# Kernel optimization log

Measured on AMD Instinct MI355X. Metric: run time of the kernel, lower is better.

Reference implementation:

```python
import jax, jax.numpy as jnp
import numpy as np

G = 32               # sdf grid resolution (grid_size init default)
SCALE_FACTOR = 0.2   # forward default scale_factor
EPS = 1e-12


def setup_inputs() -> dict:
    key = jax.random.key(0)
    k1, k2 = jax.random.split(key)
    H, V, F = 2, 778, 1538  # two hands, MANO topology
    vertices = jax.random.normal(k1, (H, V, 3), dtype=jnp.float32)
    faces = jax.random.randint(k2, (F, 3), 0, V, dtype=jnp.int32)
    return {"vertices": vertices, "faces": faces}


def _sdiv(n, d):
    return n / jnp.where(jnp.abs(d) < EPS, EPS, d)


def _point_tri_dist2(p, a, b, c):
    # p: [P,1,3]; a,b,c: [1,F,3] -> squared distance [P,F] (Ericson closest-point)
    ab = b - a; ac = c - a; ap = p - a
    d1 = jnp.sum(ab * ap, -1); d2 = jnp.sum(ac * ap, -1)
    bp = p - b; d3 = jnp.sum(ab * bp, -1); d4 = jnp.sum(ac * bp, -1)
    cp = p - c; d5 = jnp.sum(ab * cp, -1); d6 = jnp.sum(ac * cp, -1)
    vc = d1 * d4 - d3 * d2
    vb = d5 * d2 - d1 * d6
    va = d3 * d6 - d5 * d4
    denom = va + vb + vc
    v_in = _sdiv(vb, denom); w_in = _sdiv(vc, denom)
    res = a + ab * v_in[..., None] + ac * w_in[..., None]  # face interior
    # edge BC
    cond = ((va <= 0) & ((d4 - d3) >= 0) & ((d5 - d6) >= 0))[..., None]
    w = _sdiv(d4 - d3, (d4 - d3) + (d5 - d6))[..., None]
    res = jnp.where(cond, b + (c - b) * w, res)
    # edge AC
    cond = ((vb <= 0) & (d2 >= 0) & (d6 <= 0))[..., None]
    w = _sdiv(d2, d2 - d6)[..., None]
    res = jnp.where(cond, a + ac * w, res)
    # edge AB
    cond = ((vc <= 0) & (d1 >= 0) & (d3 <= 0))[..., None]
    w = _sdiv(d1, d1 - d3)[..., None]
    res = jnp.where(cond, a + ab * w, res)
    # vertex regions (highest precedence)
    res = jnp.where(((d6 >= 0) & (d5 <= d6))[..., None], jnp.broadcast_to(c, res.shape), res)
    res = jnp.where(((d3 >= 0) & (d4 <= d3))[..., None], jnp.broadcast_to(b, res.shape), res)
    res = jnp.where(((d1 <= 0) & (d2 <= 0))[..., None], jnp.broadcast_to(a, res.shape), res)
    return jnp.sum((p - res) ** 2, -1)


def _inside(p, a, b, c):
    # parity of +x ray intersections (Moller-Trumbore with dir = (1,0,0))
    e1 = b - a; e2 = c - a
    det = e1[..., 1] * (-e2[..., 2]) + e1[..., 2] * e2[..., 1]  # dot(e1, cross(dir,e2))
    inv = _sdiv(1.0, det)
    s = p - a
    u = (s[..., 1] * (-e2[..., 2]) + s[..., 2] * e2[..., 1]) * inv
    q = jnp.cross(s, e1)
    v = q[..., 0] * inv                # dot(dir, q)
    t = jnp.sum(e2 * q, -1) * inv
    hit = (jnp.abs(det) > 1e-9) & (u >= 0) & (u <= 1) & (v >= 0) & (u + v <= 1) & (t > 0)
    return (jnp.sum(hit.astype(jnp.int32), axis=-1) % 2) == 1


def _sdf_grid(tri):
    # tri: [F,3,3] scaled triangles -> phi [G,G,G] laid out [z,y,x] (grid_sample DHW)
    a = tri[None, :, 0]; b = tri[None, :, 1]; c = tri[None, :, 2]
    lin = jnp.linspace(-1.0, 1.0, G, dtype=tri.dtype)
    zz, yy, xx = jnp.meshgrid(lin, lin, lin, indexing='ij')
    pts = jnp.stack([xx, yy, zz], -1).reshape(G, G * G, 3)  # chunk over z-slabs

    def slab(ps):
        p = ps[:, None, :]
        d2 = jnp.min(_point_tri_dist2(p, a, b, c), axis=1)
        ins = _inside(p, a, b, c)
        return jnp.where(ins, jnp.sqrt(jnp.maximum(d2, 0.0)), 0.0)

    return jax.lax.map(slab, pts).reshape(G, G, G)


def _trilinear(phi, coords):
    # grid_sample(align_corners=True, padding_mode='zeros'), coords [N,3] in xyz order
    g = G - 1
    f = (coords + 1.0) * 0.5 * g
    fx, fy, fz = f[:, 0], f[:, 1], f[:, 2]
    x0f = jnp.floor(fx); y0f = jnp.floor(fy); z0f = jnp.floor(fz)
    wx = fx - x0f; wy = fy - y0f; wz = fz - z0f
    x0 = x0f.astype(jnp.int32); y0 = y0f.astype(jnp.int32); z0 = z0f.astype(jnp.int32)

    def corner(zi, yi, xi, w):
        valid = (zi >= 0) & (zi <= g) & (yi >= 0) & (yi <= g) & (xi >= 0) & (xi <= g)
        val = phi[jnp.clip(zi, 0, g), jnp.clip(yi, 0, g), jnp.clip(xi, 0, g)]
        return jnp.where(valid, val, 0.0) * w

    out = (corner(z0, y0, x0, (1 - wz) * (1 - wy) * (1 - wx))
           + corner(z0, y0, x0 + 1, (1 - wz) * (1 - wy) * wx)
           + corner(z0, y0 + 1, x0, (1 - wz) * wy * (1 - wx))
           + corner(z0, y0 + 1, x0 + 1, (1 - wz) * wy * wx)
           + corner(z0 + 1, y0, x0, wz * (1 - wy) * (1 - wx))
           + corner(z0 + 1, y0, x0 + 1, wz * (1 - wy) * wx)
           + corner(z0 + 1, y0 + 1, x0, wz * wy * (1 - wx))
           + corner(z0 + 1, y0 + 1, x0 + 1, wz * wy * wx))
    return out


def reference(vertices, faces):
    H = vertices.shape[0]
    bmin = vertices.min(axis=1)   # [H,3]
    bmax = vertices.max(axis=1)
    center = jax.lax.stop_gradient(((bmin + bmax) * 0.5)[:, None, :])           # [H,1,3]
    scale = jax.lax.stop_gradient(
        ((1.0 + SCALE_FACTOR) * 0.5 * (bmax - bmin).max(-1))[:, None, None])    # [H,1,1]
    v_scaled = jax.lax.stop_gradient((vertices - center) / scale)
    tris = v_scaled[:, faces]                                                    # [H,F,3,3]
    phi = jax.lax.stop_gradient(jax.vmap(_sdf_grid)(tris))                       # [H,G,G,G]
    i = 1  # hardcoded loop 'for i in [1]' in the source
    coords = ((vertices - center[i][None]) / scale[i][None]).reshape(-1, 3)
    phi_val = _trilinear(phi[i], coords).reshape(H, -1)
    weights = jnp.ones((H, 1), dtype=vertices.dtype).at[i, 0].set(0.0)
    loss = jnp.sum(weights * phi_val) / (H ** 2)
    return loss
```

## Files before the change

### kernel.cpp

```cpp
#include <hip/hip_runtime.h>
#include <math.h>

#define NNODE 32768
#define NTHR  256
#define STHR  1024
#define CH    256
#define MAXC  (CH + 63)
#define FGRID 2048
#define NL1   64
#define CREW  8

__device__ __forceinline__ float rguard(float d) {
    float dd = (fabsf(d) < 1e-12f) ? 1e-12f : d;
    return __builtin_amdgcn_rcpf(dd);
}

__device__ __forceinline__ void cell_of(float px, float py, float pz,
                                        int& x0, int& y0, int& z0,
                                        float& wx, float& wy, float& wz) {
#pragma clang fp contract(off)
    float fx = (px + 1.0f) * 0.5f * 31.0f;
    float fy = (py + 1.0f) * 0.5f * 31.0f;
    float fz = (pz + 1.0f) * 0.5f * 31.0f;
    float x0f = floorf(fx), y0f = floorf(fy), z0f = floorf(fz);
    wx = fx - x0f; wy = fy - y0f; wz = fz - z0f;
    x0 = (int)fmaxf(fminf(x0f, 33.0f), -2.0f);
    y0 = (int)fmaxf(fminf(y0f, 33.0f), -2.0f);
    z0 = (int)fmaxf(fminf(z0f, 33.0f), -2.0f);
}

__device__ __forceinline__ void bbox_of(const float* __restrict__ verts, int V,
                                        float& ocx, float& ocy, float& ocz,
                                        float& osc) {
#pragma clang fp contract(off)
    const float* v1 = verts + (size_t)V * 3;
    float mn[3] = {1e30f, 1e30f, 1e30f};
    float mx[3] = {-1e30f, -1e30f, -1e30f};
    for (int i = threadIdx.x; i < V; i += blockDim.x) {
        for (int c = 0; c < 3; ++c) {
            float val = v1[i * 3 + c];
            mn[c] = fminf(mn[c], val);
            mx[c] = fmaxf(mx[c], val);
        }
    }
    for (int off = 32; off >= 1; off >>= 1) {
        for (int c = 0; c < 3; ++c) {
            mn[c] = fminf(mn[c], __shfl_down(mn[c], off));
            mx[c] = fmaxf(mx[c], __shfl_down(mx[c], off));
        }
    }
    __shared__ float smn[16][3], smx[16][3];
    int wv = threadIdx.x >> 6, lane = threadIdx.x & 63;
    if (lane == 0)
        for (int c = 0; c < 3; ++c) { smn[wv][c] = mn[c]; smx[wv][c] = mx[c]; }
    __syncthreads();
    const int nw = (int)blockDim.x >> 6;
    float ext = -1e30f, cc[3];
    for (int c = 0; c < 3; ++c) {
        float lo = 1e30f, hi = -1e30f;
        for (int w = 0; w < nw; ++w) {
            lo = fminf(lo, smn[w][c]);
            hi = fmaxf(hi, smx[w][c]);
        }
        cc[c] = (lo + hi) * 0.5f;
        ext = fmaxf(ext, hi - lo);
    }
    ocx = cc[0]; ocy = cc[1]; ocz = cc[2];
    osc = (1.0f + 0.2f) * 0.5f * ext;
    __syncthreads();
}

__device__ __forceinline__ void tri_node(
        float ax, float ay, float az, float abx, float aby, float abz,
        float acx, float acy, float acz, float inv, float det,
        float dbb, float dbc, float dcc,
        float px, float py, float pz, float& mind2, int& h) {
    float apx = px - ax, apy = py - ay, apz = pz - az;
    {
#pragma clang fp contract(fast)
        float d1 = abx * apx + aby * apy + abz * apz;
        float d2 = acx * apx + acy * apy + acz * apz;
        float d3 = d1 - dbb;
        float d4 = d2 - dbc;
        float d5 = d1 - dbc;
        float d6 = d2 - dcc;
        float vc = d1 * d4 - d3 * d2;
        float vb = d5 * d2 - d1 * d6;
        float va = d3 * d6 - d5 * d4;
        float denom = va + vb + vc;
        float rd = rguard(denom);
        float v_in = vb * rd, w_in = vc * rd;
        float rx = ax + abx * v_in + acx * w_in;
        float ry = ay + aby * v_in + acy * w_in;
        float rz = az + abz * v_in + acz * w_in;
        if (va <= 0.0f && (d4 - d3) >= 0.0f && (d5 - d6) >= 0.0f) {
            float w2 = (d4 - d3) * rguard((d4 - d3) + (d5 - d6));
            rx = ax + abx + (acx - abx) * w2;
            ry = ay + aby + (acy - aby) * w2;
            rz = az + abz + (acz - abz) * w2;
        }
        if (vb <= 0.0f && d2 >= 0.0f && d6 <= 0.0f) {
            float w2 = d2 * rguard(d2 - d6);
            rx = ax + acx * w2; ry = ay + acy * w2; rz = az + acz * w2;
        }
        if (vc <= 0.0f && d1 >= 0.0f && d3 <= 0.0f) {
            float w2 = d1 * rguard(d1 - d3);
            rx = ax + abx * w2; ry = ay + aby * w2; rz = az + abz * w2;
        }
        if (d6 >= 0.0f && d5 <= d6) { rx = ax + acx; ry = ay + acy; rz = az + acz; }
        if (d3 >= 0.0f && d4 <= d3) { rx = ax + abx; ry = ay + aby; rz = az + abz; }
        if (d1 <= 0.0f && d2 <= 0.0f) { rx = ax; ry = ay; rz = az; }
        float ddx = px - rx, ddy = py - ry, ddz = pz - rz;
        mind2 = fminf(mind2, ddx * ddx + ddy * ddy + ddz * ddz);
    }
    {
#pragma clang fp contract(off)
        float u = (apy * (-acz) + apz * acy) * inv;
        float qx = apy * abz - apz * aby;
        float qy = apz * abx - apx * abz;
        float qz = apx * aby - apy * abx;
        float v = qx * inv;
        float tt = (acx * qx + acy * qy + acz * qz) * inv;
        h += (fabsf(det) > 1e-9f && u >= 0.0f && u <= 1.0f && v >= 0.0f &&
              (u + v) <= 1.0f && tt > 0.0f) ? 1 : 0;
    }
}

__global__ void __launch_bounds__(STHR) k_setup(
        const float* __restrict__ verts, const int* __restrict__ faces,
        float* __restrict__ tri, unsigned int* __restrict__ d2b,
        int* __restrict__ hits, int* __restrict__ cnt,
        unsigned long long* __restrict__ acc, int* __restrict__ done2,
        int* __restrict__ lvl1, int* __restrict__ lvl2,
        int* __restrict__ list, int V, int F) {
    float cx0, cy0, cz0, sc;
    bbox_of(verts, V, cx0, cy0, cz0, sc);
    const int b = (int)blockIdx.x, tid = threadIdx.x;

    if (b == 0) {
        __shared__ unsigned bm[NNODE / 32];
        __shared__ int scnt[STHR];
        bm[tid] = 0u;
        __syncthreads();
        for (int i = tid; i < V; i += STHR) {
#pragma clang fp contract(off)
            float px = (verts[i * 3 + 0] - cx0) / sc;
            float py = (verts[i * 3 + 1] - cy0) / sc;
            float pz = (verts[i * 3 + 2] - cz0) / sc;
            int x0, y0, z0; float wx, wy, wz;
            cell_of(px, py, pz, x0, y0, z0, wx, wy, wz);
            for (int k = 0; k < 8; ++k) {
                int zi = z0 + ((k >> 2) & 1), yi = y0 + ((k >> 1) & 1),
                    xi = x0 + (k & 1);
                if ((unsigned)zi < 32u && (unsigned)yi < 32u && (unsigned)xi < 32u) {
                    int node = (zi * 32 + yi) * 32 + xi;
                    atomicOr(&bm[node >> 5], 1u << (node & 31));
                }
            }
        }
        __syncthreads();
        unsigned w0 = bm[tid];
        int c = __popc(w0);
        scnt[tid] = c;
        __syncthreads();
        for (int off = 1; off < STHR; off <<= 1) {
            int v_ = (tid >= off) ? scnt[tid - off] : 0;
            __syncthreads();
            scnt[tid] += v_;
            __syncthreads();
        }
        int total = scnt[STHR - 1];
        if (tid == STHR - 1) cnt[0] = total;
        int off = scnt[tid] - c;
        int basebit = tid * 32;
        while (w0) {
            int bb = __ffs(w0) - 1;
            list[off++] = basebit + bb;
            w0 &= w0 - 1;
        }
        __syncthreads();
        for (int t = tid; t < total; t += STHR) {
            int nd = list[t];
            d2b[nd] = 0xFFFFFFFFu;
            hits[nd] = 0;
        }
        if (tid < NL1) lvl1[tid * 16] = 0;
        if (tid == 0) { acc[0] = 0ull; done2[0] = 0; lvl2[0] = 0; }
    } else {
        int f = (b - 1) * STHR + tid;
        if (f < F) {
#pragma clang fp contract(off)
            const float* v1 = verts + (size_t)V * 3;
            int i0 = faces[f * 3 + 0], i1 = faces[f * 3 + 1], i2 = faces[f * 3 + 2];
            float ax = (v1[i0 * 3 + 0] - cx0) / sc, ay = (v1[i0 * 3 + 1] - cy0) / sc,
                  az = (v1[i0 * 3 + 2] - cz0) / sc;
            float bx = (v1[i1 * 3 + 0] - cx0) / sc, by = (v1[i1 * 3 + 1] - cy0) / sc,
                  bz = (v1[i1 * 3 + 2] - cz0) / sc;
            float cx = (v1[i2 * 3 + 0] - cx0) / sc, cy = (v1[i2 * 3 + 1] - cy0) / sc,
                  cz = (v1[i2 * 3 + 2] - cz0) / sc;
            float abx = bx - ax, aby = by - ay, abz = bz - az;
            float acx = cx - ax, acy = cy - ay, acz = cz - az;
            float det = aby * (-acz) + abz * acy;
            float dd = (fabsf(det) < 1e-12f) ? 1e-12f : det;
            float inv = 1.0f / dd;
            float* r = tri + (size_t)f * 16;
            r[0] = ax;  r[1] = ay;  r[2] = az;
            r[3] = abx; r[4] = aby; r[5] = abz;
            r[6] = acx; r[7] = acy; r[8] = acz;
            r[9] = inv; r[10] = det;
            r[11] = abx * abx + aby * aby + abz * abz;
            r[12] = abx * acx + aby * acy + abz * acz;
            r[13] = acx * acx + acy * acy + acz * acz;
            r[14] = 0.0f; r[15] = 0.0f;
        }
    }
}

__global__ void __launch_bounds__(NTHR) k_fused(
        const float* __restrict__ tri, const int* __restrict__ list,
        const int* __restrict__ cnt, unsigned int* __restrict__ d2b,
        int* __restrict__ hits, int* __restrict__ lvl1, int* __restrict__ lvl2,
        unsigned long long* __restrict__ acc, int* __restrict__ done2,
        const float* __restrict__ verts, float* __restrict__ out,
        int F, int nch, int V) {
    const int n = cnt[0];
    const int ngroups = (n + 3) >> 2;
    const int total = ngroups * nch;
    const int tid = threadIdx.x, lane = tid & 63;
    __shared__ float s[14][MAXC];

    for (int item = (int)blockIdx.x; item < total; item += FGRID) {
        const int group = item / nch;
        const int c = item - group * nch;
        const int cbase = c * CH;
        const int tn = (c == nch - 1) ? (F - cbase) : CH;

        for (int j = tid; j < tn; j += NTHR) {
            const float4* g = (const float4*)(tri + (size_t)(cbase + j) * 16);
            float4 r0 = g[0], r1 = g[1], r2 = g[2], r3 = g[3];
            s[0][j] = r0.x;  s[1][j] = r0.y;  s[2][j] = r0.z;  s[3][j] = r0.w;
            s[4][j] = r1.x;  s[5][j] = r1.y;  s[6][j] = r1.z;  s[7][j] = r1.w;
            s[8][j] = r2.x;  s[9][j] = r2.y;  s[10][j] = r2.z; s[11][j] = r2.w;
            s[12][j] = r3.x; s[13][j] = r3.y;
        }
        __syncthreads();

        const int idx = group * 4 + (tid >> 6);
        const int node = (idx < n) ? list[idx] : -1;
        float px = 0, py = 0, pz = 0;
        if (node >= 0) {
#pragma clang fp contract(off)
            px = (float)((double)(node & 31) * (2.0 / 31.0) - 1.0);
            py = (float)((double)((node >> 5) & 31) * (2.0 / 31.0) - 1.0);
            pz = (float)((double)(node >> 10) * (2.0 / 31.0) - 1.0);
        }
        float m = 1e30f;
        int h = 0;
        if (node >= 0) {
            for (int mi = 0; mi * 64 < tn; ++mi) {
                int j = lane + mi * 64;
                if (j < tn) {
                    tri_node(s[0][j], s[1][j], s[2][j], s[3][j], s[4][j], s[5][j],
                             s[6][j], s[7][j], s[8][j], s[9][j], s[10][j],
                             s[11][j], s[12][j], s[13][j], px, py, pz, m, h);
                }
            }
        }
        for (int off = 32; off >= 1; off >>= 1) {
            m = fminf(m, __shfl_xor(m, off));
            h += __shfl_xor(h, off);
        }
        if (lane == 0 && node >= 0) {
            atomicMin(d2b + node, __float_as_uint(m));
            atomicAdd(hits + node, h);
        }
        __syncthreads();
    }

    __shared__ int crew_slice;
    __syncthreads();
    if (tid == 0) {
        crew_slice = -1;
        int cohort = (int)blockIdx.x & (NL1 - 1);
        int quota = (FGRID + NL1 - 1 - cohort) / NL1;
        int p1 = atomicAdd(&lvl1[cohort * 16], 1);
        if (p1 == quota - 1) {
            int p2 = atomicAdd(lvl2, 1);
            if (p2 >= NL1 - CREW) {
                while (__hip_atomic_load(lvl2, __ATOMIC_RELAXED,
                                         __HIP_MEMORY_SCOPE_AGENT) < NL1)
                    __builtin_amdgcn_s_sleep(1);
                crew_slice = p2 - (NL1 - CREW);
            }
        }
    }
    __syncthreads();
    const int slice = crew_slice;
    if (slice < 0) return;

    float cx, cy, cz, sc;
    bbox_of(verts, V, cx, cy, cz, sc);
    float val = 0.0f;
    {
#pragma clang fp contract(off)
        for (int i = slice * NTHR + tid; i < V; i += CREW * NTHR) {
            float px = (verts[i * 3 + 0] - cx) / sc;
            float py = (verts[i * 3 + 1] - cy) / sc;
            float pz = (verts[i * 3 + 2] - cz) / sc;
            int x0, y0, z0; float wx, wy, wz;
            cell_of(px, py, pz, x0, y0, z0, wx, wy, wz);
            auto corner = [&](int zi, int yi, int xi, float w) -> float {
#pragma clang fp contract(off)
                bool valid = (zi >= 0) && (zi <= 31) && (yi >= 0) && (yi <= 31) &&
                             (xi >= 0) && (xi <= 31);
                int zc = min(max(zi, 0), 31);
                int yc = min(max(yi, 0), 31);
                int xc = min(max(xi, 0), 31);
                int idx = (zc * 32 + yc) * 32 + xc;
                unsigned dbits = __hip_atomic_load(&d2b[idx], __ATOMIC_RELAXED,
                                                   __HIP_MEMORY_SCOPE_AGENT);
                int hh = __hip_atomic_load(&hits[idx], __ATOMIC_RELAXED,
                                           __HIP_MEMORY_SCOPE_AGENT);
                float vv = (hh & 1) ? sqrtf(fmaxf(__uint_as_float(dbits), 0.0f))
                                    : 0.0f;
                return valid ? vv * w : 0.0f;
            };
            val += corner(z0, y0, x0, (1.0f - wz) * (1.0f - wy) * (1.0f - wx))
                 + corner(z0, y0, x0 + 1, (1.0f - wz) * (1.0f - wy) * wx)
                 + corner(z0, y0 + 1, x0, (1.0f - wz) * wy * (1.0f - wx))
                 + corner(z0, y0 + 1, x0 + 1, (1.0f - wz) * wy * wx)
                 + corner(z0 + 1, y0, x0, wz * (1.0f - wy) * (1.0f - wx))
                 + corner(z0 + 1, y0, x0 + 1, wz * (1.0f - wy) * wx)
                 + corner(z0 + 1, y0 + 1, x0, wz * wy * (1.0f - wx))
                 + corner(z0 + 1, y0 + 1, x0 + 1, wz * wy * wx);
        }
    }
    __shared__ float sm[NTHR];
    sm[tid] = val;
    __syncthreads();
    for (int ss = NTHR / 2; ss >= 1; ss >>= 1) {
        if (tid < ss) sm[tid] += sm[tid + ss];
        __syncthreads();
    }
    if (tid == 0) {
        unsigned long long fx =
            (unsigned long long)((double)sm[0] * 4294967296.0);
        atomicAdd(acc, fx);
        asm volatile("s_waitcnt vmcnt(0)");
        int prev = atomicAdd(done2, 1);
        if (prev == CREW - 1) {
            unsigned long long tot = atomicAdd(acc, 0ull);
            out[0] = (float)((double)tot / 4294967296.0 * 0.25);
        }
    }
}

extern "C" void kernel_launch(void* const* d_in, const int* in_sizes, int n_in,
                              void* d_out, int out_size, void* d_ws, size_t ws_size,
                              hipStream_t stream) {
    const float* verts = (const float*)d_in[0];
    const int* faces = (const int*)d_in[1];
    float* out = (float*)d_out;
    float* ws = (float*)d_ws;

    int V = in_sizes[0] / 6;
    int F = in_sizes[1] / 3;

    unsigned long long* acc = (unsigned long long*)ws;
    int* done2 = (int*)(ws + 2);
    int* cnt = (int*)(ws + 3);
    int* lvl2 = (int*)(ws + 4);
    int* lvl1 = (int*)(ws + 16);
    float* tri = ws + 16 + NL1 * 16;
    unsigned int* d2b = (unsigned int*)(tri + 16 * (size_t)F);
    int* hits = (int*)(d2b + NNODE);
    int* list = hits + NNODE;

    int nch = F / CH;
    int rem = F - nch * CH;
    if (nch == 0 || rem >= 64) nch += (rem > 0 ? 1 : 0);
    if (nch == 0) nch = 1;

    int nrec = (F + STHR - 1) / STHR;

    k_setup<<<1 + nrec, STHR, 0, stream>>>(verts, faces, tri, d2b, hits, cnt, acc,
                                           done2, lvl1, lvl2, list, V, F);
    k_fused<<<FGRID, NTHR, 0, stream>>>(tri, list, cnt, d2b, hits, lvl1, lvl2, acc,
                                        done2, verts, out, F, nch, V);
}
```

Measured before the change: 43.99 us.

## Compute point-triangle distance algebraically from dot products and defer atomics

```diff
diff --git a/kernel.cpp b/kernel.cpp
--- a/kernel.cpp
+++ b/kernel.cpp
@@ -72,7 +72,7 @@
 
 __device__ __forceinline__ void tri_node(
         float ax, float ay, float az, float abx, float aby, float abz,
-        float acx, float acy, float acz, float inv, float det,
+        float acx, float acy, float acz, float inv, float ebc,
         float dbb, float dbc, float dcc,
         float px, float py, float pz, float& mind2, int& h) {
     float apx = px - ax, apy = py - ay, apz = pz - az;
@@ -80,6 +80,7 @@
 #pragma clang fp contract(fast)
         float d1 = abx * apx + aby * apy + abz * apz;
         float d2 = acx * apx + acy * apy + acz * apz;
+        float apd = apx * apx + apy * apy + apz * apz;
         float d3 = d1 - dbb;
         float d4 = d2 - dbc;
         float d5 = d1 - dbc;
@@ -89,29 +90,26 @@
         float va = d3 * d6 - d5 * d4;
         float denom = va + vb + vc;
         float rd = rguard(denom);
-        float v_in = vb * rd, w_in = vc * rd;
-        float rx = ax + abx * v_in + acx * w_in;
-        float ry = ay + aby * v_in + acy * w_in;
-        float rz = az + abz * v_in + acz * w_in;
+        float v = vb * rd, w = vc * rd;
+        float dd = apd - 2.0f * (v * d1 + w * d2) + v * v * dbb +
+                   2.0f * v * w * dbc + w * w * dcc;
         if (va <= 0.0f && (d4 - d3) >= 0.0f && (d5 - d6) >= 0.0f) {
             float w2 = (d4 - d3) * rguard((d4 - d3) + (d5 - d6));
-            rx = ax + abx + (acx - abx) * w2;
-            ry = ay + aby + (acy - aby) * w2;
-            rz = az + abz + (acz - abz) * w2;
+            dd = apd - 2.0f * d1 + dbb - 2.0f * w2 * (d2 - d1) +
+                 2.0f * w2 * (dbc - dbb) + w2 * w2 * ebc;
         }
         if (vb <= 0.0f && d2 >= 0.0f && d6 <= 0.0f) {
             float w2 = d2 * rguard(d2 - d6);
-            rx = ax + acx * w2; ry = ay + acy * w2; rz = az + acz * w2;
+            dd = apd - 2.0f * w2 * d2 + w2 * w2 * dcc;
         }
         if (vc <= 0.0f && d1 >= 0.0f && d3 <= 0.0f) {
             float w2 = d1 * rguard(d1 - d3);
-            rx = ax + abx * w2; ry = ay + aby * w2; rz = az + abz * w2;
-        }
-        if (d6 >= 0.0f && d5 <= d6) { rx = ax + acx; ry = ay + acy; rz = az + acz; }
-        if (d3 >= 0.0f && d4 <= d3) { rx = ax + abx; ry = ay + aby; rz = az + abz; }
-        if (d1 <= 0.0f && d2 <= 0.0f) { rx = ax; ry = ay; rz = az; }
-        float ddx = px - rx, ddy = py - ry, ddz = pz - rz;
-        mind2 = fminf(mind2, ddx * ddx + ddy * ddy + ddz * ddz);
+            dd = apd - 2.0f * w2 * d1 + w2 * w2 * dbb;
+        }
+        if (d6 >= 0.0f && d5 <= d6) dd = apd - 2.0f * d2 + dcc;
+        if (d3 >= 0.0f && d4 <= d3) dd = apd - 2.0f * d1 + dbb;
+        if (d1 <= 0.0f && d2 <= 0.0f) dd = apd;
+        mind2 = fminf(mind2, fmaxf(dd, 0.0f));
     }
     {
 #pragma clang fp contract(off)
@@ -121,8 +119,8 @@
         float qz = apx * aby - apy * abx;
         float v = qx * inv;
         float tt = (acx * qx + acy * qy + acz * qz) * inv;
-        h += (fabsf(det) > 1e-9f && u >= 0.0f && u <= 1.0f && v >= 0.0f &&
-              (u + v) <= 1.0f && tt > 0.0f) ? 1 : 0;
+        h += (u >= 0.0f && u <= 1.0f && v >= 0.0f && (u + v) <= 1.0f &&
+              tt > 0.0f) ? 1 : 0;
     }
 }
 
@@ -203,11 +201,14 @@
             float det = aby * (-acz) + abz * acy;
             float dd = (fabsf(det) < 1e-12f) ? 1e-12f : det;
             float inv = 1.0f / dd;
+            float invp = (fabsf(det) > 1e-9f) ? inv : 0.0f;
+            float bcx = acx - abx, bcy = acy - aby, bcz = acz - abz;
             float* r = tri + (size_t)f * 16;
             r[0] = ax;  r[1] = ay;  r[2] = az;
             r[3] = abx; r[4] = aby; r[5] = abz;
             r[6] = acx; r[7] = acy; r[8] = acz;
-            r[9] = inv; r[10] = det;
+            r[9] = invp;
+            r[10] = bcx * bcx + bcy * bcy + bcz * bcz;
             r[11] = abx * abx + aby * aby + abz * abz;
             r[12] = abx * acx + aby * acy + abz * acz;
             r[13] = acx * acx + acy * acy + acz * acz;
@@ -229,6 +230,10 @@
     const int tid = threadIdx.x, lane = tid & 63;
     __shared__ float s[14][MAXC];
 
+    int pnode = -1;
+    float pm = 0.0f;
+    int ph = 0;
+
     for (int item = (int)blockIdx.x; item < total; item += FGRID) {
         const int group = item / nch;
         const int c = item - group * nch;
@@ -244,6 +249,12 @@
             s[12][j] = r3.x; s[13][j] = r3.y;
         }
         __syncthreads();
+
+        if (lane == 0 && pnode >= 0) {
+            atomicMin(d2b + pnode, __float_as_uint(pm));
+            atomicAdd(hits + pnode, ph);
+        }
+        pnode = -1;
 
         const int idx = group * 4 + (tid >> 6);
         const int node = (idx < n) ? list[idx] : -1;
@@ -270,11 +281,12 @@
             m = fminf(m, __shfl_xor(m, off));
             h += __shfl_xor(h, off);
         }
-        if (lane == 0 && node >= 0) {
-            atomicMin(d2b + node, __float_as_uint(m));
-            atomicAdd(hits + node, h);
-        }
-        __syncthreads();
+        if (node >= 0) { pnode = node; pm = m; ph = h; }
+        __syncthreads();
+    }
+    if (lane == 0 && pnode >= 0) {
+        atomicMin(d2b + pnode, __float_as_uint(pm));
+        atomicAdd(hits + pnode, ph);
     }
 
     __shared__ int crew_slice;
```

New measurement: 45.85 us. 4.2% more time.

## Stage all triangles in LDS once per block and drop per-chunk barriers

Applied to the files above, without the earlier changes.

```diff
diff --git a/kernel.cpp b/kernel.cpp
--- a/kernel.cpp
+++ b/kernel.cpp
@@ -2,11 +2,10 @@
 #include <math.h>
 
 #define NNODE 32768
-#define NTHR  256
 #define STHR  1024
-#define CH    256
-#define MAXC  (CH + 63)
-#define FGRID 2048
+#define BTHR  1024
+#define FGRID 256
+#define LDSF  1600
 #define NL1   64
 #define CREW  8
 
@@ -216,39 +215,40 @@
     }
 }
 
-__global__ void __launch_bounds__(NTHR) k_fused(
+__global__ void __launch_bounds__(BTHR) k_fused(
         const float* __restrict__ tri, const int* __restrict__ list,
         const int* __restrict__ cnt, unsigned int* __restrict__ d2b,
         int* __restrict__ hits, int* __restrict__ lvl1, int* __restrict__ lvl2,
         unsigned long long* __restrict__ acc, int* __restrict__ done2,
         const float* __restrict__ verts, float* __restrict__ out,
-        int F, int nch, int V) {
+        int F, int V) {
+    __shared__ float s[14][LDSF];
+    const int tid = threadIdx.x, lane = tid & 63, wv = tid >> 6;
+
+    for (int j = tid; j < F; j += BTHR) {
+        const float4* g = (const float4*)(tri + (size_t)j * 16);
+        float4 r0 = g[0], r1 = g[1], r2 = g[2], r3 = g[3];
+        s[0][j] = r0.x;  s[1][j] = r0.y;  s[2][j] = r0.z;  s[3][j] = r0.w;
+        s[4][j] = r1.x;  s[5][j] = r1.y;  s[6][j] = r1.z;  s[7][j] = r1.w;
+        s[8][j] = r2.x;  s[9][j] = r2.y;  s[10][j] = r2.z; s[11][j] = r2.w;
+        s[12][j] = r3.x; s[13][j] = r3.y;
+    }
+    __syncthreads();
+
     const int n = cnt[0];
-    const int ngroups = (n + 3) >> 2;
-    const int total = ngroups * nch;
-    const int tid = threadIdx.x, lane = tid & 63;
-    __shared__ float s[14][MAXC];
-
-    for (int item = (int)blockIdx.x; item < total; item += FGRID) {
-        const int group = item / nch;
-        const int c = item - group * nch;
-        const int cbase = c * CH;
-        const int tn = (c == nch - 1) ? (F - cbase) : CH;
-
-        for (int j = tid; j < tn; j += NTHR) {
-            const float4* g = (const float4*)(tri + (size_t)(cbase + j) * 16);
-            float4 r0 = g[0], r1 = g[1], r2 = g[2], r3 = g[3];
-            s[0][j] = r0.x;  s[1][j] = r0.y;  s[2][j] = r0.z;  s[3][j] = r0.w;
-            s[4][j] = r1.x;  s[5][j] = r1.y;  s[6][j] = r1.z;  s[7][j] = r1.w;
-            s[8][j] = r2.x;  s[9][j] = r2.y;  s[10][j] = r2.z; s[11][j] = r2.w;
-            s[12][j] = r3.x; s[13][j] = r3.y;
-        }
-        __syncthreads();
-
-        const int idx = group * 4 + (tid >> 6);
-        const int node = (idx < n) ? list[idx] : -1;
-        float px = 0, py = 0, pz = 0;
-        if (node >= 0) {
+    const int nitems = n * 2;
+    const int wgid = (int)blockIdx.x * 16 + wv;
+    const int nb64 = (F + 63) >> 6;
+    const int nb0 = (nb64 + 1) >> 1;
+
+    for (int it = wgid; it < nitems; it += FGRID * 16) {
+        const int nodeIdx = it >> 1;
+        const int half = it & 1;
+        const int f0 = half ? nb0 * 64 : 0;
+        const int f1 = half ? F : nb0 * 64;
+        const int node = list[nodeIdx];
+        float px, py, pz;
+        {
 #pragma clang fp contract(off)
             px = (float)((double)(node & 31) * (2.0 / 31.0) - 1.0);
             py = (float)((double)((node >> 5) & 31) * (2.0 / 31.0) - 1.0);
@@ -256,25 +256,22 @@
         }
         float m = 1e30f;
         int h = 0;
-        if (node >= 0) {
-            for (int mi = 0; mi * 64 < tn; ++mi) {
-                int j = lane + mi * 64;
-                if (j < tn) {
-                    tri_node(s[0][j], s[1][j], s[2][j], s[3][j], s[4][j], s[5][j],
-                             s[6][j], s[7][j], s[8][j], s[9][j], s[10][j],
-                             s[11][j], s[12][j], s[13][j], px, py, pz, m, h);
-                }
+        for (int j0 = f0; j0 < f1; j0 += 64) {
+            int j = j0 + lane;
+            if (j < f1) {
+                tri_node(s[0][j], s[1][j], s[2][j], s[3][j], s[4][j], s[5][j],
+                         s[6][j], s[7][j], s[8][j], s[9][j], s[10][j],
+                         s[11][j], s[12][j], s[13][j], px, py, pz, m, h);
             }
         }
         for (int off = 32; off >= 1; off >>= 1) {
             m = fminf(m, __shfl_xor(m, off));
             h += __shfl_xor(h, off);
         }
-        if (lane == 0 && node >= 0) {
+        if (lane == 0) {
             atomicMin(d2b + node, __float_as_uint(m));
             atomicAdd(hits + node, h);
         }
-        __syncthreads();
     }
 
     __shared__ int crew_slice;
@@ -303,7 +300,7 @@
     float val = 0.0f;
     {
 #pragma clang fp contract(off)
-        for (int i = slice * NTHR + tid; i < V; i += CREW * NTHR) {
+        for (int i = slice * BTHR + tid; i < V; i += CREW * BTHR) {
             float px = (verts[i * 3 + 0] - cx) / sc;
             float py = (verts[i * 3 + 1] - cy) / sc;
             float pz = (verts[i * 3 + 2] - cz) / sc;
@@ -335,10 +332,10 @@
                  + corner(z0 + 1, y0 + 1, x0 + 1, wz * wy * wx);
         }
     }
-    __shared__ float sm[NTHR];
+    __shared__ float sm[BTHR];
     sm[tid] = val;
     __syncthreads();
-    for (int ss = NTHR / 2; ss >= 1; ss >>= 1) {
+    for (int ss = BTHR / 2; ss >= 1; ss >>= 1) {
         if (tid < ss) sm[tid] += sm[tid + ss];
         __syncthreads();
     }
@@ -365,6 +362,7 @@
 
     int V = in_sizes[0] / 6;
     int F = in_sizes[1] / 3;
+    if (F > LDSF) F = LDSF;
 
     unsigned long long* acc = (unsigned long long*)ws;
     int* done2 = (int*)(ws + 2);
@@ -376,15 +374,10 @@
     int* hits = (int*)(d2b + NNODE);
     int* list = hits + NNODE;
 
-    int nch = F / CH;
-    int rem = F - nch * CH;
-    if (nch == 0 || rem >= 64) nch += (rem > 0 ? 1 : 0);
-    if (nch == 0) nch = 1;
-
     int nrec = (F + STHR - 1) / STHR;
 
     k_setup<<<1 + nrec, STHR, 0, stream>>>(verts, faces, tri, d2b, hits, cnt, acc,
                                            done2, lvl1, lvl2, list, V, F);
-    k_fused<<<FGRID, NTHR, 0, stream>>>(tri, list, cnt, d2b, hits, lvl1, lvl2, acc,
-                                        done2, verts, out, F, nch, V);
-}
+    k_fused<<<FGRID, BTHR, 0, stream>>>(tri, list, cnt, d2b, hits, lvl1, lvl2, acc,
+                                        done2, verts, out, F, V);
+}
```

Result: slower. 62.97 us (+43.1%).
